# Optimization experiments

Hardware: AMD Instinct MI355X
Metric: run time of the kernel (lower is better)

## Reference

```python
import jax, jax.numpy as jnp
import numpy as np

DIM_IN = 512
DIM_HEAD = 64
HEADS = 8
KV_HEADS = 2
CONTEXT_LEN = 4096
B, N = 4, 2048


def setup_inputs() -> dict:
    key = jax.random.key(0)
    ks = jax.random.split(key, 6)
    s = 1.0 / np.sqrt(DIM_IN)
    return {
        "x": jax.random.normal(ks[0], (B, DIM_IN, N), dtype=jnp.float32),
        "gamma": jnp.ones((DIM_IN,), jnp.float32),
        "beta": jnp.zeros((DIM_IN,), jnp.float32),
        "Wq": jax.random.normal(ks[1], (DIM_IN, DIM_HEAD * HEADS), jnp.float32) * s,
        "Wkv": jax.random.normal(ks[2], (DIM_IN, DIM_HEAD * KV_HEADS * 2), jnp.float32) * s,
        "Wout": jax.random.normal(ks[3], (DIM_HEAD * HEADS, DIM_IN), jnp.float32) * (1.0 / np.sqrt(DIM_HEAD * HEADS)),
        "bout": jnp.zeros((DIM_IN,), jnp.float32),
    }


def _rotate_half(t):
    t1, t2 = jnp.split(t, 2, axis=-1)
    return jnp.concatenate([-t2, t1], axis=-1)


def _xpos_rotary(q, k, n, dim_head, scale_base):
    # lucidrains-style xPos rotary embedding
    pos = jnp.arange(n, dtype=jnp.float32)
    inv_freq = 1.0 / (10000.0 ** (jnp.arange(0, dim_head, 2, dtype=jnp.float32) / dim_head))
    freqs = pos[:, None] * inv_freq[None, :]            # (n, dh/2)
    freqs = jnp.concatenate([freqs, freqs], axis=-1)    # (n, dh)
    base_scale = (jnp.arange(0, dim_head, 2, dtype=jnp.float32) + 0.4 * dim_head) / (1.4 * dim_head)
    power = (pos - n // 2) / scale_base                 # (n,)
    scale = base_scale[None, :] ** power[:, None]       # (n, dh/2)
    scale = jnp.concatenate([scale, scale], axis=-1)    # (n, dh)
    cos, sin = jnp.cos(freqs), jnp.sin(freqs)
    q = (q * cos + _rotate_half(q) * sin) * scale
    k = (k * cos + _rotate_half(k) * sin) / scale
    return q, k


def reference(x, gamma, beta, Wq, Wkv, Wout, bout):
    b, d, n = x.shape
    h, kvh, dh = HEADS, KV_HEADS, DIM_HEAD
    xt = jnp.swapaxes(x, 1, 2)                           # (b, n, d)
    mu = jnp.mean(xt, axis=-1, keepdims=True)
    var = jnp.mean((xt - mu) ** 2, axis=-1, keepdims=True)
    xn = (xt - mu) * jax.lax.rsqrt(var + 1e-5) * gamma + beta
    q = (xn @ Wq).reshape(b, n, h, dh).transpose(0, 2, 1, 3)      # (b, h, n, dh)
    kv = xn @ Wkv
    k, v = jnp.split(kv, 2, axis=-1)
    k = k.reshape(b, n, kvh, dh).transpose(0, 2, 1, 3)            # (b, kvh, n, dh)
    v = v.reshape(b, n, kvh, dh).transpose(0, 2, 1, 3)
    r = h // kvh
    # repeat 'b h n d -> b (r h) n d': tile whole kv-head block r times
    k = jnp.tile(k, (1, r, 1, 1))
    v = jnp.tile(v, (1, r, 1, 1))
    q, k = _xpos_rotary(q, k, n, dh, CONTEXT_LEN)
    scores = jnp.einsum("bhqd,bhkd->bhqk", q, k) * (1.0 / np.sqrt(dh))
    attn = jax.nn.softmax(scores, axis=-1)
    out = jnp.einsum("bhqk,bhkd->bhqd", attn, v)                  # (b, h, n, dh)
    out = out.transpose(0, 2, 1, 3).reshape(b, n, h * dh)
    y = xn + out @ Wout + bout                                    # residual uses normed x
    return jnp.swapaxes(y, 1, 2)                                  # (b, d, n)
```

## Files before the change

kernel.cpp:

```cpp
#include <hip/hip_runtime.h>
#include <stdint.h>

#define DIM 512
#define DH  64
#define NH  8
#define NKV 2
#define NB  4
#define NS  2048
#define TAB (NS*32)

typedef __attribute__((ext_vector_type(8))) short short8;
typedef __attribute__((ext_vector_type(4))) short s16x4;
typedef __attribute__((ext_vector_type(4))) float f32x4;
typedef __attribute__((ext_vector_type(16))) float f32x16;
typedef __attribute__((ext_vector_type(2))) unsigned uint2v;
typedef __attribute__((ext_vector_type(4))) unsigned uint4v;

__device__ __forceinline__ unsigned short f2bf(float f) {
  union { float f; unsigned u; } v; v.f = f;
  return (unsigned short)((v.u + 0x7fffu + ((v.u >> 16) & 1u)) >> 16);
}
__device__ __forceinline__ float bf2f(unsigned short b) {
  union { unsigned u; float f; } v; v.u = ((unsigned)b) << 16;
  return v.f;
}
__device__ __forceinline__ unsigned cvt_pk_bf16(float a, float b) {
  unsigned r;
  asm("v_cvt_pk_bf16_f32 %0, %1, %2" : "=v"(r) : "v"(a), "v"(b));
  return r;
}
__device__ __forceinline__ float exp2_raw(float x) {
  float r;
  asm("v_exp_f32 %0, %1" : "=v"(r) : "v"(x));
  return r;
}
__device__ __forceinline__ float rcp_raw(float x) {
  float r;
  asm("v_rcp_f32 %0, %1" : "=v"(r) : "v"(x));
  return r;
}
__device__ __forceinline__ short8 merge8(short8 a, short8 b, float rl) {
  uint4v u;
  #pragma unroll
  for (int i = 0; i < 4; ++i) {
    float x0 = (bf2f((unsigned short)a[2*i])   + bf2f((unsigned short)b[2*i]))   * rl;
    float x1 = (bf2f((unsigned short)a[2*i+1]) + bf2f((unsigned short)b[2*i+1])) * rl;
    u[i] = cvt_pk_bf16(x0, x1);
  }
  return __builtin_bit_cast(short8, u);
}

__global__ __launch_bounds__(256) void lnprep_kernel(const float* __restrict__ x,
    const float* __restrict__ gamma, const float* __restrict__ beta,
    const float* __restrict__ Wq, const float* __restrict__ Wkv, const float* __restrict__ Wout,
    unsigned short* __restrict__ xn, unsigned short* __restrict__ Wqkvt,
    unsigned short* __restrict__ Woutt, float* __restrict__ tabs) {
  __shared__ float t[64][65];
  const int gid = blockIdx.x;
  const int tid = threadIdx.x;
  if (gid < 256) {
    const int b = gid >> 6;
    const int n0 = (gid & 63) * 32;
    const int nl = tid & 31, grp = tid >> 5;
    const float* xb = x + (size_t)b * DIM * NS + (size_t)grp * 64 * NS + n0 + nl;
    float v[64];
    float s = 0.f, s2 = 0.f;
    #pragma unroll
    for (int i = 0; i < 64; ++i) {
      v[i] = xb[(size_t)i * NS];
      s += v[i]; s2 += v[i] * v[i];
    }
    float* sm = &t[0][0];
    float* sq = &t[8][0];
    float* mu_s = &t[16][0];
    float* rs_s = &t[17][0];
    sm[grp*32 + nl] = s; sq[grp*32 + nl] = s2;
    __syncthreads();
    if (tid < 32) {
      float ts = 0.f, ts2 = 0.f;
      #pragma unroll
      for (int g = 0; g < 8; ++g) { ts += sm[g*32 + tid]; ts2 += sq[g*32 + tid]; }
      float mu = ts * (1.f/512.f);
      float var = ts2 * (1.f/512.f) - mu*mu;
      mu_s[tid] = mu; rs_s[tid] = rsqrtf(var + 1e-5f);
    }
    __syncthreads();
    const float mu = mu_s[nl], rs = rs_s[nl];
    unsigned short* dst = &xn[((size_t)(b*NS + n0 + nl))*DIM + grp*64];
    #pragma unroll
    for (int c = 0; c < 8; ++c) {
      short8 o;
      #pragma unroll
      for (int j = 0; j < 8; ++j) {
        int d = grp*64 + c*8 + j;
        o[j] = (short)f2bf((v[c*8 + j] - mu) * rs * gamma[d] + beta[d]);
      }
      *(short8*)&dst[c*8] = o;
    }
    return;
  }
  const int id = gid - 256;
  if (id >= 160) {
    int base = (id - 160) * 256 + tid;
    #pragma unroll 4
    for (int ii = 0; ii < 32; ++ii) {
      int tix = base + ii * 2048;
      int pos = tix >> 5, i = tix & 31;
      float inv = exp2f(-(float)i * (13.287712379549449f / 32.f));
      float ang = (float)pos * inv;
      float sv, cv; sincosf(ang, &sv, &cv);
      float bse = ((float)(2*i) + 25.6f) / 89.6f;
      float power = ((float)pos - 1024.f) / 4096.f;
      float sc = exp2f(power * log2f(bse));
      tabs[tix]         = cv;
      tabs[TAB + tix]   = sv;
      tabs[2*TAB + tix] = sc * 0.125f * 1.4426950408889634f;
      tabs[3*TAB + tix] = 1.f / sc;
    }
    return;
  }
  const float* src; int W, k0, c0; unsigned short* dst; int drow0;
  if (id < 64)      { src = Wq;  W = 512; k0 = (id>>3)*64;        c0 = (id&7)*64;        dst = Wqkvt; drow0 = c0; }
  else if (id < 96) { int i2 = id-64; src = Wkv; W = 256; k0 = (i2>>2)*64; c0 = (i2&3)*64; dst = Wqkvt; drow0 = 512 + c0; }
  else              { int i3 = id-96; src = Wout; W = 512; k0 = (i3>>3)*64; c0 = (i3&7)*64; dst = Woutt; drow0 = c0; }
  #pragma unroll 4
  for (int it = 0; it < 16; ++it) {
    int row = it*4 + (tid>>6), col = tid & 63;
    t[row][col] = src[(size_t)(k0+row)*W + c0 + col];
  }
  __syncthreads();
  #pragma unroll 4
  for (int it = 0; it < 16; ++it) {
    int row = it*4 + (tid>>6), col = tid & 63;
    dst[(size_t)(drow0 + row)*512 + k0 + col] = f2bf(t[col][row]);
  }
}

__global__ __launch_bounds__(256, 3) void qkv_kernel(const unsigned short* __restrict__ A,
    const unsigned short* __restrict__ Bt, const float* __restrict__ tabs,
    unsigned short* __restrict__ q, unsigned short* __restrict__ k,
    unsigned short* __restrict__ v) {
  __shared__ __align__(16) short As[2][64][40];
  __shared__ __align__(16) short Bs[2][128][40];
  const int m0 = blockIdx.x * 64, ntile = blockIdx.y, n0 = ntile * 128;
  const int tid = threadIdx.x, w = tid >> 6, lane = tid & 63;
  const int wr = w >> 1, wc = w & 1;
  f32x4 acc[2][4];
  #pragma unroll
  for (int i = 0; i < 2; ++i)
    #pragma unroll
    for (int j = 0; j < 4; ++j) acc[i][j] = (f32x4){0.f,0.f,0.f,0.f};
  const int rA = tid >> 2, c8 = (tid & 3) * 8;
  const unsigned short* Ar0 = &A[(size_t)(m0 + rA)*DIM + c8];
  const unsigned short* Br0 = &Bt[(size_t)(n0 + rA)*DIM + c8];
  const unsigned short* Br1 = &Bt[(size_t)(n0 + 64 + rA)*DIM + c8];
  *(short8*)&As[0][rA][c8]      = *(const short8*)Ar0;
  *(short8*)&Bs[0][rA][c8]      = *(const short8*)Br0;
  *(short8*)&Bs[0][64 + rA][c8] = *(const short8*)Br1;
  short8 pa0 = *(const short8*)(Ar0 + 32);
  short8 pb0 = *(const short8*)(Br0 + 32);
  short8 pb1 = *(const short8*)(Br1 + 32);
  __syncthreads();
  for (int t = 0; t < 16; ++t) {
    const int cur = t & 1;
    short8 af[2], bfr[4];
    #pragma unroll
    for (int mf = 0; mf < 2; ++mf)
      af[mf] = *(const short8*)&As[cur][wr*32 + mf*16 + (lane & 15)][(lane >> 4)*8];
    #pragma unroll
    for (int nf = 0; nf < 4; ++nf)
      bfr[nf] = *(const short8*)&Bs[cur][wc*64 + nf*16 + (lane & 15)][(lane >> 4)*8];
    __builtin_amdgcn_s_setprio(1);
    #pragma unroll
    for (int mf = 0; mf < 2; ++mf)
      #pragma unroll
      for (int nf = 0; nf < 4; ++nf)
        acc[mf][nf] = __builtin_amdgcn_mfma_f32_16x16x32_bf16(af[mf], bfr[nf], acc[mf][nf], 0, 0, 0);
    __builtin_amdgcn_s_setprio(0);
    if (t < 15) {
      *(short8*)&As[cur^1][rA][c8]      = pa0;
      *(short8*)&Bs[cur^1][rA][c8]      = pb0;
      *(short8*)&Bs[cur^1][64 + rA][c8] = pb1;
      if (t < 14) {
        const int kc = (t + 2) * 32;
        pa0 = *(const short8*)(Ar0 + kc);
        pb0 = *(const short8*)(Br0 + kc);
        pb1 = *(const short8*)(Br1 + kc);
      }
      __syncthreads();
    }
  }
  const int mw = m0 + wr*32, cw = n0 + wc*64;
  if (ntile < 4) {
    #pragma unroll
    for (int nfp = 0; nfp < 2; ++nfp) {
      const int c_lo = cw + nfp*16 + (lane & 15);
      const int head = c_lo >> 6, ii = c_lo & 31;
      const float* tb = tabs + ii;
      #pragma unroll
      for (int mf = 0; mf < 2; ++mf) {
        #pragma unroll
        for (int r = 0; r < 4; ++r) {
          int mm = mw + mf*16 + (lane >> 4)*4 + r;
          int bb = mm >> 11, n = mm & (NS-1);
          float cv = tb[n*32], sv = tb[TAB + n*32], qs = tb[2*TAB + n*32];
          float lo = acc[mf][nfp][r], hi = acc[mf][nfp+2][r];
          size_t base = (((size_t)bb*NH + head)*NS + n)*DH;
          q[base + ii]      = f2bf((lo*cv - hi*sv)*qs);
          q[base + ii + 32] = f2bf((hi*cv + lo*sv)*qs);
        }
      }
    }
  } else if (ntile == 4) {
    #pragma unroll
    for (int nfp = 0; nfp < 2; ++nfp) {
      const int c_lo = cw + nfp*16 + (lane & 15);
      const int kvh = (c_lo - 512) >> 6, ii = c_lo & 31;
      const float* tb = tabs + ii;
      #pragma unroll
      for (int mf = 0; mf < 2; ++mf) {
        #pragma unroll
        for (int r = 0; r < 4; ++r) {
          int mm = mw + mf*16 + (lane >> 4)*4 + r;
          int bb = mm >> 11, n = mm & (NS-1);
          float cv = tb[n*32], sv = tb[TAB + n*32], ks = tb[3*TAB + n*32];
          float lo = acc[mf][nfp][r], hi = acc[mf][nfp+2][r];
          size_t base = (((size_t)bb*NKV + kvh)*NS + n)*DH;
          k[base + ii]      = f2bf((lo*cv - hi*sv)*ks);
          k[base + ii + 32] = f2bf((hi*cv + lo*sv)*ks);
        }
      }
    }
  } else {
    #pragma unroll
    for (int nf = 0; nf < 4; ++nf) {
      const int c = cw + nf*16 + (lane & 15);
      const int rel = c - 640;
      const int kvh = rel >> 6, dd = rel & 63;
      #pragma unroll
      for (int mf = 0; mf < 2; ++mf) {
        int mm = mw + mf*16 + (lane >> 4)*4;
        int bb = mm >> 11, n = mm & (NS-1);
        s16x4 sv4;
        #pragma unroll
        for (int r = 0; r < 4; ++r) sv4[r] = (short)f2bf(acc[mf][nf][r]);
        *(s16x4*)&v[(((size_t)bb*NKV + kvh)*DH + dd)*NS + n] = sv4;
      }
    }
  }
}

__global__ __launch_bounds__(512, 2) void attn_kernel(const unsigned short* __restrict__ q,
    const unsigned short* __restrict__ kg, const unsigned short* __restrict__ vtp,
    unsigned short* __restrict__ op0, unsigned short* __restrict__ op1,
    float* __restrict__ lp) {
  __shared__ __align__(16) short kt[2][64][72];
  __shared__ __align__(16) short vt[2][64][72];
  const int bid = blockIdx.x;
  const int dsr = (bid & 7) * 64 + (bid >> 3);
  const int qt   = dsr & 7;
  const int half = (dsr >> 3) & 1;
  const int bh   = dsr >> 4;
  const int h = bh & 7, b = bh >> 3;
  const int kvh = h & (NKV-1);
  const int q0 = qt * 256;
  const int tid = threadIdx.x, w = tid >> 6, lane = tid & 63;
  const int l31 = lane & 31, hf = lane >> 5;
  short8 q8[4];
  const unsigned short* qp = q + (((size_t)b*NH + h)*NS + q0 + w*32 + l31)*DH + hf*8;
  #pragma unroll
  for (int s = 0; s < 4; ++s) q8[s] = *(const short8*)(qp + s*16);
  const unsigned short* kb = kg + ((size_t)b*NKV + kvh)*NS*DH;
  const unsigned short* vb = vtp + ((size_t)b*NKV + kvh)*DH*NS;
  const int kbase = half * 1024;
  const int srow = tid >> 3, scol = (tid & 7) * 8;
  *(short8*)&kt[0][srow][scol] = *(const short8*)&kb[(size_t)(kbase + srow)*DH + scol];
  *(short8*)&vt[0][srow][scol] = *(const short8*)&vb[(size_t)srow*NS + kbase + scol];
  short8 kr = *(const short8*)&kb[(size_t)(kbase + 64 + srow)*DH + scol];
  short8 vr = *(const short8*)&vb[(size_t)srow*NS + kbase + 64 + scol];
  f32x16 o0 = {}, o1 = {};
  float lsum = 0.f;
  __syncthreads();
  for (int t = 0; t < 16; ++t) {
    const int cur = t & 1;
    short8 kf0[4], kf1[4];
    #pragma unroll
    for (int s = 0; s < 4; ++s) {
      kf0[s] = *(const short8*)&kt[cur][l31][s*16 + hf*8];
      kf1[s] = *(const short8*)&kt[cur][32 + l31][s*16 + hf*8];
    }
    f32x16 st0 = {}, st1 = {};
    __builtin_amdgcn_s_setprio(1);
    #pragma unroll
    for (int s = 0; s < 4; ++s) {
      st0 = __builtin_amdgcn_mfma_f32_32x32x16_bf16(kf0[s], q8[s], st0, 0, 0, 0);
      st1 = __builtin_amdgcn_mfma_f32_32x32x16_bf16(kf1[s], q8[s], st1, 0, 0, 0);
    }
    __builtin_amdgcn_s_setprio(0);
    float p0[16], p1[16];
    #pragma unroll
    for (int r = 0; r < 16; ++r) {
      p0[r] = exp2_raw(st0[r]);
      p1[r] = exp2_raw(st1[r]);
      lsum += p0[r] + p1[r];
    }
    short8 paf[4];
    #pragma unroll
    for (int t2 = 0; t2 < 2; ++t2) {
      const float* pp = t2 ? p1 : p0;
      #pragma unroll
      for (int w16 = 0; w16 < 2; ++w16) {
        const int rb = w16*8;
        unsigned x = cvt_pk_bf16(pp[rb+0], pp[rb+1]);
        unsigned z = cvt_pk_bf16(pp[rb+2], pp[rb+3]);
        unsigned y = cvt_pk_bf16(pp[rb+4], pp[rb+5]);
        unsigned u = cvt_pk_bf16(pp[rb+6], pp[rb+7]);
        uint2v r1 = __builtin_amdgcn_permlane32_swap(x, y, false, false);
        uint2v r2 = __builtin_amdgcn_permlane32_swap(z, u, false, false);
        uint4v pk4;
        pk4[0] = r1[0]; pk4[1] = r2[0]; pk4[2] = r1[1]; pk4[3] = r2[1];
        paf[t2*2 + w16] = __builtin_bit_cast(short8, pk4);
      }
    }
    __builtin_amdgcn_s_setprio(1);
    #pragma unroll
    for (int kwin = 0; kwin < 4; ++kwin) {
      short8 vf0 = *(const short8*)&vt[cur][l31][kwin*16 + hf*8];
      short8 vf1 = *(const short8*)&vt[cur][32 + l31][kwin*16 + hf*8];
      o0 = __builtin_amdgcn_mfma_f32_32x32x16_bf16(paf[kwin], vf0, o0, 0, 0, 0);
      o1 = __builtin_amdgcn_mfma_f32_32x32x16_bf16(paf[kwin], vf1, o1, 0, 0, 0);
    }
    __builtin_amdgcn_s_setprio(0);
    if (t < 15) {
      *(short8*)&kt[cur^1][srow][scol] = kr;
      *(short8*)&vt[cur^1][srow][scol] = vr;
      if (t < 14) {
        const int k2 = kbase + (t + 2) * 64;
        kr = *(const short8*)&kb[(size_t)(k2 + srow)*DH + scol];
        vr = *(const short8*)&vb[(size_t)srow*NS + k2 + scol];
      }
      __syncthreads();
    }
  }
  lsum += __shfl_xor(lsum, 32);
  if (hf == 0)
    lp[(size_t)half*NB*NH*NS + ((size_t)b*NH + h)*NS + q0 + w*32 + l31] = lsum;
  unsigned short* op = half ? op1 : op0;
  #pragma unroll
  for (int r = 0; r < 16; ++r) {
    const int ql = (r & 3) + 8*(r >> 2) + 4*hf;
    const int n = q0 + w*32 + ql;
    unsigned short* aor = &op[((size_t)b*NS + n)*DIM + h*DH + l31];
    aor[0]  = f2bf(o0[r]);
    aor[32] = f2bf(o1[r]);
  }
}

__global__ __launch_bounds__(256, 3) void out_kernel(const unsigned short* __restrict__ op0,
    const unsigned short* __restrict__ op1, const float* __restrict__ lp,
    const unsigned short* __restrict__ Bt, const unsigned short* __restrict__ xn,
    const float* __restrict__ bout, float* __restrict__ out) {
  __shared__ __align__(16) short As[2][64][40];
  __shared__ __align__(16) short Bs[2][128][40];
  const int m0 = blockIdx.x * 64, n0 = blockIdx.y * 128;
  const int tid = threadIdx.x, w = tid >> 6, lane = tid & 63;
  const int wr = w >> 1, wc = w & 1;
  f32x4 acc[2][4];
  #pragma unroll
  for (int i = 0; i < 2; ++i)
    #pragma unroll
    for (int j = 0; j < 4; ++j) acc[i][j] = (f32x4){0.f,0.f,0.f,0.f};
  const int rA = tid >> 2, c8 = (tid & 3) * 8;
  const int rowm = m0 + rA;
  const int b0 = rowm >> 11, nn0 = rowm & (NS-1);
  const float* lp0 = lp + ((size_t)b0*NH)*NS + nn0;
  const float* lp1 = lp0 + (size_t)NB*NH*NS;
  const unsigned short* A0 = &op0[(size_t)rowm*DIM + c8];
  const unsigned short* A1 = &op1[(size_t)rowm*DIM + c8];
  const unsigned short* Br0 = &Bt[(size_t)(n0 + rA)*DIM + c8];
  const unsigned short* Br1 = &Bt[(size_t)(n0 + 64 + rA)*DIM + c8];
  float rlc = rcp_raw(lp0[0] + lp1[0]);
  *(short8*)&As[0][rA][c8]      = merge8(*(const short8*)A0, *(const short8*)A1, rlc);
  *(short8*)&Bs[0][rA][c8]      = *(const short8*)Br0;
  *(short8*)&Bs[0][64 + rA][c8] = *(const short8*)Br1;
  short8 pa0 = *(const short8*)(A0 + 32);
  short8 pa1 = *(const short8*)(A1 + 32);
  float rlp = rlc;
  short8 pb0 = *(const short8*)(Br0 + 32);
  short8 pb1 = *(const short8*)(Br1 + 32);
  __syncthreads();
  for (int t = 0; t < 16; ++t) {
    const int cur = t & 1;
    short8 af[2], bfr[4];
    #pragma unroll
    for (int mf = 0; mf < 2; ++mf)
      af[mf] = *(const short8*)&As[cur][wr*32 + mf*16 + (lane & 15)][(lane >> 4)*8];
    #pragma unroll
    for (int nf = 0; nf < 4; ++nf)
      bfr[nf] = *(const short8*)&Bs[cur][wc*64 + nf*16 + (lane & 15)][(lane >> 4)*8];
    __builtin_amdgcn_s_setprio(1);
    #pragma unroll
    for (int mf = 0; mf < 2; ++mf)
      #pragma unroll
      for (int nf = 0; nf < 4; ++nf)
        acc[mf][nf] = __builtin_amdgcn_mfma_f32_16x16x32_bf16(af[mf], bfr[nf], acc[mf][nf], 0, 0, 0);
    __builtin_amdgcn_s_setprio(0);
    if (t < 15) {
      *(short8*)&As[cur^1][rA][c8]      = merge8(pa0, pa1, rlp);
      *(short8*)&Bs[cur^1][rA][c8]      = pb0;
      *(short8*)&Bs[cur^1][64 + rA][c8] = pb1;
      if (t < 14) {
        const int kc = (t + 2) * 32;
        pa0 = *(const short8*)(A0 + kc);
        pa1 = *(const short8*)(A1 + kc);
        pb0 = *(const short8*)(Br0 + kc);
        pb1 = *(const short8*)(Br1 + kc);
        const int h2 = (t + 2) >> 1;
        rlp = rcp_raw(lp0[h2*NS] + lp1[h2*NS]);
      }
      __syncthreads();
    }
  }
  const int mw = m0 + wr*32, cw = n0 + wc*64;
  #pragma unroll
  for (int nf = 0; nf < 4; ++nf) {
    const int d = cw + nf*16 + (lane & 15);
    const float bo = bout[d];
    #pragma unroll
    for (int mf = 0; mf < 2; ++mf) {
      const int mb = mw + mf*16 + (lane >> 4)*4;
      const int bb = mb >> 11, n = mb & (NS-1);
      f32x4 res;
      #pragma unroll
      for (int r = 0; r < 4; ++r)
        res[r] = acc[mf][nf][r] + bf2f(xn[(size_t)(mb + r)*DIM + d]) + bo;
      *(f32x4*)&out[((size_t)bb*DIM + d)*NS + n] = res;
    }
  }
}

extern "C" void kernel_launch(void* const* d_in, const int* in_sizes, int n_in,
                              void* d_out, int out_size, void* d_ws, size_t ws_size,
                              hipStream_t stream) {
  (void)in_sizes; (void)n_in; (void)out_size; (void)ws_size;
  const float* x     = (const float*)d_in[0];
  const float* gamma = (const float*)d_in[1];
  const float* beta  = (const float*)d_in[2];
  const float* Wq    = (const float*)d_in[3];
  const float* Wkv   = (const float*)d_in[4];
  const float* Wout  = (const float*)d_in[5];
  const float* bout  = (const float*)d_in[6];
  float* out = (float*)d_out;
  char* ws = (char*)d_ws;
  unsigned short* xn    = (unsigned short*)(ws);
  unsigned short* qb    = (unsigned short*)(ws + (size_t)(8<<20));
  unsigned short* kb    = (unsigned short*)(ws + (size_t)(16<<20));
  unsigned short* vb    = (unsigned short*)(ws + (size_t)(18<<20));
  unsigned short* op0   = (unsigned short*)(ws + (size_t)(20<<20));
  unsigned short* op1   = (unsigned short*)(ws + (size_t)(28<<20));
  unsigned short* wqkvt = (unsigned short*)(ws + (size_t)(36<<20));
  unsigned short* woutt = (unsigned short*)(ws + (size_t)(36<<20) + 786432);
  float* tabs           = (float*)(ws + (size_t)(36<<20) + 786432 + 524288);
  float* lp             = (float*)(ws + (size_t)(36<<20) + 786432 + 524288 + 1048576);

  lnprep_kernel<<<dim3(424), dim3(256), 0, stream>>>(x, gamma, beta, Wq, Wkv, Wout,
                                                     xn, wqkvt, woutt, tabs);
  qkv_kernel<<<dim3(128, 6), dim3(256), 0, stream>>>(xn, wqkvt, tabs, qb, kb, vb);
  attn_kernel<<<dim3(512), dim3(512), 0, stream>>>(qb, kb, vb, op0, op1, lp);
  out_kernel<<<dim3(128, 4), dim3(256), 0, stream>>>(op0, op1, lp, woutt, xn, bout, out);
}
```

Before: 85.34 us.

## Store V in MFMA fragment order and load directly to registers

```diff
diff --git a/kernel.cpp b/kernel.cpp
--- a/kernel.cpp
+++ b/kernel.cpp
@@ -237,25 +237,28 @@
       const int c = cw + nf*16 + (lane & 15);
       const int rel = c - 640;
       const int kvh = rel >> 6, dd = rel & 63;
+      const int dh2 = dd >> 5, l31v = dd & 31;
       #pragma unroll
       for (int mf = 0; mf < 2; ++mf) {
         int mm = mw + mf*16 + (lane >> 4)*4;
         int bb = mm >> 11, n = mm & (NS-1);
+        const int hb = bb*NKV + kvh;
         s16x4 sv4;
         #pragma unroll
         for (int r = 0; r < 4; ++r) sv4[r] = (short)f2bf(acc[mf][nf][r]);
-        *(s16x4*)&v[(((size_t)bb*NKV + kvh)*DH + dd)*NS + n] = sv4;
+        size_t idx = (((((size_t)hb*32 + (n >> 6))*2 + dh2)*4 + ((n >> 4) & 3))*64
+                     + ((n >> 3) & 1)*32 + l31v)*8 + (n & 7);
+        *(s16x4*)&v[idx] = sv4;
       }
     }
   }
 }
 
 __global__ __launch_bounds__(512, 2) void attn_kernel(const unsigned short* __restrict__ q,
-    const unsigned short* __restrict__ kg, const unsigned short* __restrict__ vtp,
+    const unsigned short* __restrict__ kg, const unsigned short* __restrict__ vfb,
     unsigned short* __restrict__ op0, unsigned short* __restrict__ op1,
     float* __restrict__ lp) {
   __shared__ __align__(16) short kt[2][64][72];
-  __shared__ __align__(16) short vt[2][64][72];
   const int bid = blockIdx.x;
   const int dsr = (bid & 7) * 64 + (bid >> 3);
   const int qt   = dsr & 7;
@@ -263,6 +266,7 @@
   const int bh   = dsr >> 4;
   const int h = bh & 7, b = bh >> 3;
   const int kvh = h & (NKV-1);
+  const int hb = b*NKV + kvh;
   const int q0 = qt * 256;
   const int tid = threadIdx.x, w = tid >> 6, lane = tid & 63;
   const int l31 = lane & 31, hf = lane >> 5;
@@ -271,24 +275,26 @@
   #pragma unroll
   for (int s = 0; s < 4; ++s) q8[s] = *(const short8*)(qp + s*16);
   const unsigned short* kb = kg + ((size_t)b*NKV + kvh)*NS*DH;
-  const unsigned short* vb = vtp + ((size_t)b*NKV + kvh)*DH*NS;
+  const unsigned short* vf_base = vfb + ((size_t)hb*32 + half*16)*4096 + lane*8;
   const int kbase = half * 1024;
   const int srow = tid >> 3, scol = (tid & 7) * 8;
   *(short8*)&kt[0][srow][scol] = *(const short8*)&kb[(size_t)(kbase + srow)*DH + scol];
-  *(short8*)&vt[0][srow][scol] = *(const short8*)&vb[(size_t)srow*NS + kbase + scol];
   short8 kr = *(const short8*)&kb[(size_t)(kbase + 64 + srow)*DH + scol];
-  short8 vr = *(const short8*)&vb[(size_t)srow*NS + kbase + 64 + scol];
   f32x16 o0 = {}, o1 = {};
   float lsum = 0.f;
   __syncthreads();
   for (int t = 0; t < 16; ++t) {
     const int cur = t & 1;
+    const unsigned short* vc = vf_base + (size_t)t*4096;
     short8 kf0[4], kf1[4];
     #pragma unroll
     for (int s = 0; s < 4; ++s) {
       kf0[s] = *(const short8*)&kt[cur][l31][s*16 + hf*8];
       kf1[s] = *(const short8*)&kt[cur][32 + l31][s*16 + hf*8];
     }
+    short8 vf0[4];
+    #pragma unroll
+    for (int kw = 0; kw < 4; ++kw) vf0[kw] = *(const short8*)(vc + kw*512);
     f32x16 st0 = {}, st1 = {};
     __builtin_amdgcn_s_setprio(1);
     #pragma unroll
@@ -322,22 +328,22 @@
         paf[t2*2 + w16] = __builtin_bit_cast(short8, pk4);
       }
     }
+    short8 vf1[4];
+    #pragma unroll
+    for (int kw = 0; kw < 4; ++kw) vf1[kw] = *(const short8*)(vc + (4 + kw)*512);
     __builtin_amdgcn_s_setprio(1);
     #pragma unroll
-    for (int kwin = 0; kwin < 4; ++kwin) {
-      short8 vf0 = *(const short8*)&vt[cur][l31][kwin*16 + hf*8];
-      short8 vf1 = *(const short8*)&vt[cur][32 + l31][kwin*16 + hf*8];
-      o0 = __builtin_amdgcn_mfma_f32_32x32x16_bf16(paf[kwin], vf0, o0, 0, 0, 0);
-      o1 = __builtin_amdgcn_mfma_f32_32x32x16_bf16(paf[kwin], vf1, o1, 0, 0, 0);
-    }
+    for (int kw = 0; kw < 4; ++kw)
+      o0 = __builtin_amdgcn_mfma_f32_32x32x16_bf16(paf[kw], vf0[kw], o0, 0, 0, 0);
+    #pragma unroll
+    for (int kw = 0; kw < 4; ++kw)
+      o1 = __builtin_amdgcn_mfma_f32_32x32x16_bf16(paf[kw], vf1[kw], o1, 0, 0, 0);
     __builtin_amdgcn_s_setprio(0);
     if (t < 15) {
       *(short8*)&kt[cur^1][srow][scol] = kr;
-      *(short8*)&vt[cur^1][srow][scol] = vr;
       if (t < 14) {
         const int k2 = kbase + (t + 2) * 64;
         kr = *(const short8*)&kb[(size_t)(k2 + srow)*DH + scol];
-        vr = *(const short8*)&vb[(size_t)srow*NS + k2 + scol];
       }
       __syncthreads();
     }
@@ -455,7 +461,7 @@
   unsigned short* xn    = (unsigned short*)(ws);
   unsigned short* qb    = (unsigned short*)(ws + (size_t)(8<<20));
   unsigned short* kb    = (unsigned short*)(ws + (size_t)(16<<20));
-  unsigned short* vb    = (unsigned short*)(ws + (size_t)(18<<20));
+  unsigned short* vfb   = (unsigned short*)(ws + (size_t)(18<<20));
   unsigned short* op0   = (unsigned short*)(ws + (size_t)(20<<20));
   unsigned short* op1   = (unsigned short*)(ws + (size_t)(28<<20));
   unsigned short* wqkvt = (unsigned short*)(ws + (size_t)(36<<20));
@@ -465,7 +471,7 @@
 
   lnprep_kernel<<<dim3(424), dim3(256), 0, stream>>>(x, gamma, beta, Wq, Wkv, Wout,
                                                      xn, wqkvt, woutt, tabs);
-  qkv_kernel<<<dim3(128, 6), dim3(256), 0, stream>>>(xn, wqkvt, tabs, qb, kb, vb);
-  attn_kernel<<<dim3(512), dim3(512), 0, stream>>>(qb, kb, vb, op0, op1, lp);
+  qkv_kernel<<<dim3(128, 6), dim3(256), 0, stream>>>(xn, wqkvt, tabs, qb, kb, vfb);
+  attn_kernel<<<dim3(512), dim3(512), 0, stream>>>(qb, kb, vfb, op0, op1, lp);
   out_kernel<<<dim3(128, 4), dim3(256), 0, stream>>>(op0, op1, lp, woutt, xn, bout, out);
 }
```

After: 89.03 us. +4.3%, slower.
